# Performance work log

Measured on AMD Instinct MI355X. Metric: run time of the kernel, lower is better.

Reference implementation:

```python
import jax, jax.numpy as jnp
from jax import lax
import numpy as np

B, N = 32, 16384
C, K = 64, 21
T = 30
L = 10.0
LAM = 0.1


def setup_inputs() -> dict:
    key = jax.random.key(0)
    k1, k2 = jax.random.split(key)
    y = jax.random.normal(k1, (B, 1, N), dtype=jnp.float32)
    H = jax.random.normal(k2, (C, 1, K), dtype=jnp.float32)
    H = H / jnp.linalg.norm(H, axis=-1, keepdims=True)  # F.normalize(p=2, dim=-1)
    return {"y": y, "H": H}


def _conv(y, H):
    # torch F.conv1d(y [B,1,N], H [C,1,K]) -> [B,C,N-K+1] (cross-correlation)
    return lax.conv_general_dilated(y, H, (1,), 'VALID',
                                    dimension_numbers=('NCH', 'OIH', 'NCH'))


def _convT(x, H):
    # torch F.conv_transpose1d(x [B,C,M], H [C,1,K]) -> [B,1,M+K-1]
    k = H.shape[-1]
    Ht = jnp.transpose(jnp.flip(H, -1), (1, 0, 2))  # [1,C,K] OIH, flipped
    return lax.conv_general_dilated(x, Ht, (1,), [(k - 1, k - 1)],
                                    dimension_numbers=('NCH', 'OIH', 'NCH'))


def reference(y, H):
    enc_dim = y.shape[-1] - H.shape[-1] + 1  # N - K + 1
    b = y.shape[0]
    c = H.shape[0]
    x0 = jnp.zeros((b, c, enc_dim), dtype=y.dtype)
    s0 = jnp.asarray(1.0, dtype=y.dtype)

    def step(carry, _):
        x_old, x_tmp, s_old = carry
        res = y - _convT(x_tmp, H)                      # residual [B,1,N]
        x_new = x_tmp + _conv(res, H) / L               # gradient step
        x_new = jax.nn.relu(x_new - LAM / L)            # soft-threshold (nonneg)
        s_new = (1.0 + jnp.sqrt(1.0 + 4.0 * s_old * s_old)) / 2.0
        x_tmp_next = x_new + (s_old - 1.0) / s_new * (x_new - x_old)
        return (x_new, x_tmp_next, s_new), None

    (x_new, _, _), _ = lax.scan(step, (x0, x0, s0), None, length=T)
    y_hat = _convT(x_new, H)
    return (y_hat, x_new)
```

## Files before the change

kernel.cpp:

```cpp
#include <hip/hip_runtime.h>
#include <math.h>

#define B_ 32
#define N_ 16384
#define K_ 21
#define C_ 64
#define M_ (N_ - K_ + 1)
#define T_ 30

#define TILE 236
#define NBLK 70
#define UPW  256
#define NT   256

__global__ __launch_bounds__(NT) void fused_step4_kernel(
    const float* __restrict__ Xc, const float* __restrict__ Xo,
    float* __restrict__ Xw,
    const float* __restrict__ Ut, const float* __restrict__ Uo,
    float* __restrict__ Uw,
    const float* __restrict__ y, const float* __restrict__ Hg,
    const float bp, const float bm, const int first)
{
  __shared__ float rs[280];
  __shared__ float rp[4][256];

  const int tid = threadIdx.x;
  const int wv  = tid >> 6;
  const int l   = tid & 63;
  const int b   = blockIdx.y;
  const int x   = blockIdx.x;
  const int m0  = x * TILE;
  const bool has_o = (bm != 0.f);

  if (tid < 24) rs[256 + tid] = 0.f;

  {
    const int n = m0 + tid;
    float r = 0.f;
    if (n < N_) {
      r = y[(size_t)b * N_ + n];
      if (!first) {
        const float* Ub = Ut + (size_t)b * NBLK * UPW;
        float ut;
        if (tid >= 236) {
          ut = Ub[(x + 1) * UPW + tid - 236] + Ub[x * UPW + tid];
        } else {
          ut = Ub[x * UPW + tid];
          if (tid < 20 && x > 0) ut += Ub[(x - 1) * UPW + 236 + tid];
        }
        r -= bp * ut;
        if (has_o) {
          const float* Vb = Uo + (size_t)b * NBLK * UPW;
          float uo;
          if (tid >= 236) {
            uo = Vb[(x + 1) * UPW + tid - 236] + Vb[x * UPW + tid];
          } else {
            uo = Vb[x * UPW + tid];
            if (tid < 20 && x > 0) uo += Vb[(x - 1) * UPW + 236 + tid];
          }
          r -= bm * uo;
        }
      }
    }
    rs[tid] = r;
  }
  __syncthreads();

  float wr[24];
  #pragma unroll
  for (int kk = 0; kk < 6; ++kk) {
    const float4 v = *(const float4*)&rs[(l << 2) + (kk << 2)];
    wr[4*kk+0] = v.x; wr[4*kk+1] = v.y;
    wr[4*kk+2] = v.z; wr[4*kk+3] = v.w;
  }

  const int  mown = m0 + (l << 2);
  const int  coff = (mown <= M_ - 4) ? mown : (M_ - 4);
  const bool act  = (l < 59) && ((l << 2) < M_ - m0);
  const size_t bC = (size_t)b * C_;

  float p0 = 0.f, p1 = 0.f, p2 = 0.f, p3 = 0.f;

  for (int k = 0; k < 4; ++k) {
    #pragma unroll
    for (int j = 0; j < 4; ++j) {
      const int cg = __builtin_amdgcn_readfirstlane((k << 4) + (wv << 2) + j);
      const float* hc = Hg + cg * K_;

      float g0 = 0.f, g1 = 0.f, g2 = 0.f, g3 = 0.f;
      #pragma unroll
      for (int u = 0; u < 21; ++u) {
        const float hv = hc[u];
        g0 = fmaf(wr[u],     hv, g0);
        g1 = fmaf(wr[u + 1], hv, g1);
        g2 = fmaf(wr[u + 2], hv, g2);
        g3 = fmaf(wr[u + 3], hv, g3);
      }

      float xt0 = 0.f, xt1 = 0.f, xt2 = 0.f, xt3 = 0.f;
      if (!first) {
        const float4 a = *(const float4*)(Xc + (bC + cg) * M_ + coff);
        float ox = 0.f, oy = 0.f, oz = 0.f, ow = 0.f;
        if (has_o) {
          const float4 o = *(const float4*)(Xo + (bC + cg) * M_ + coff);
          ox = o.x; oy = o.y; oz = o.z; ow = o.w;
        }
        xt0 = fmaf(bm, ox, bp * a.x);
        xt1 = fmaf(bm, oy, bp * a.y);
        xt2 = fmaf(bm, oz, bp * a.z);
        xt3 = fmaf(bm, ow, bp * a.w);
      }

      float o0 = fmaxf(fmaf(g0, 0.1f, xt0) - 0.01f, 0.f);
      float o1 = fmaxf(fmaf(g1, 0.1f, xt1) - 0.01f, 0.f);
      float o2 = fmaxf(fmaf(g2, 0.1f, xt2) - 0.01f, 0.f);
      float o3 = fmaxf(fmaf(g3, 0.1f, xt3) - 0.01f, 0.f);
      if (!act) { o0 = 0.f; o1 = 0.f; o2 = 0.f; o3 = 0.f; }
      if (act)
        *(float4*)(Xw + (bC + cg) * M_ + mown) = make_float4(o0, o1, o2, o3);

      float w[24];
      w[20] = o0; w[21] = o1; w[22] = o2; w[23] = o3;
      #pragma unroll
      for (int d = 0; d < 5; ++d) {
        const int src = l - 5 + d;
        w[4*d+0] = __shfl(o0, src);
        w[4*d+1] = __shfl(o1, src);
        w[4*d+2] = __shfl(o2, src);
        w[4*d+3] = __shfl(o3, src);
      }

      #pragma unroll
      for (int u = 0; u < 21; ++u) {
        const float hv = hc[20 - u];
        p0 = fmaf(w[u],     hv, p0);
        p1 = fmaf(w[u + 1], hv, p1);
        p2 = fmaf(w[u + 2], hv, p2);
        p3 = fmaf(w[u + 3], hv, p3);
      }
    }
  }

  rp[wv][(l<<2)+0] = p0; rp[wv][(l<<2)+1] = p1;
  rp[wv][(l<<2)+2] = p2; rp[wv][(l<<2)+3] = p3;
  __syncthreads();

  Uw[((size_t)b * NBLK + x) * UPW + tid] =
      rp[0][tid] + rp[1][tid] + rp[2][tid] + rp[3][tid];
}

__global__ __launch_bounds__(NT) void yhat_combine_kernel(
    const float* __restrict__ Uw, float* __restrict__ outy)
{
  const int tid = threadIdx.x;
  const int n = blockIdx.x * 256 + tid;
  const int b = blockIdx.y;
  const int x = n / 236;
  const int i = n - x * 236;
  const float* Ub = Uw + (size_t)b * NBLK * UPW;
  float v = Ub[x * UPW + i];
  if (i < 20 && x > 0) v += Ub[(x - 1) * UPW + 236 + i];
  outy[(size_t)b * N_ + n] = v;
}

#define XWID 276
#define Q4PC 69
#define NQ4  (16 * Q4PC)

__global__ __launch_bounds__(NT, 4) void fused_step_r5_kernel(
    const float* __restrict__ Xc, const float* __restrict__ Xo,
    float* __restrict__ Xw, const float* __restrict__ y,
    const float* __restrict__ Hg, const float bp, const float bm,
    const int first)
{
  __shared__ float xs[16][XWID];
  __shared__ float rp[4][256];
  __shared__ float rs[256];

  const int tid = threadIdx.x;
  const int wv  = tid >> 6;
  const int l   = tid & 63;
  const int b   = blockIdx.y;
  const int m0  = blockIdx.x * TILE;
  const int g0  = m0 - 20;
  const bool has_o = (bm != 0.f);

  if (!first) {
    float p0 = 0.f, p1 = 0.f, p2 = 0.f, p3 = 0.f;
    for (int k = 0; k < 4; ++k) {
      const int ch0 = k << 4;
      const float* pcb = Xc + ((size_t)b * C_ + ch0) * M_;
      const float* pob = Xo + ((size_t)b * C_ + ch0) * M_;
      __syncthreads();
      for (int f = tid; f < NQ4; f += NT) {
        const int c  = f / Q4PC;
        const int i4 = f - c * Q4PC;
        const int g  = g0 + (i4 << 2);
        const float* pa = pcb + (size_t)c * M_ + g;
        const float* pb = pob + (size_t)c * M_ + g;
        float ax, ay, az, aw, ox, oy, oz, ow;
        if (g >= 0 && g + 3 < M_) {
          const float4 a = *(const float4*)pa;
          ax = a.x; ay = a.y; az = a.z; aw = a.w;
          if (has_o) {
            const float4 o = *(const float4*)pb;
            ox = o.x; oy = o.y; oz = o.z; ow = o.w;
          } else { ox = oy = oz = ow = 0.f; }
        } else {
          ax = ay = az = aw = ox = oy = oz = ow = 0.f;
          if ((unsigned)(g+0) < (unsigned)M_) { ax = pa[0]; if (has_o) ox = pb[0]; }
          if ((unsigned)(g+1) < (unsigned)M_) { ay = pa[1]; if (has_o) oy = pb[1]; }
          if ((unsigned)(g+2) < (unsigned)M_) { az = pa[2]; if (has_o) oz = pb[2]; }
          if ((unsigned)(g+3) < (unsigned)M_) { aw = pa[3]; if (has_o) ow = pb[3]; }
        }
        float4 w4;
        w4.x = fmaf(bm, ox, bp * ax);
        w4.y = fmaf(bm, oy, bp * ay);
        w4.z = fmaf(bm, oz, bp * az);
        w4.w = fmaf(bm, ow, bp * aw);
        *(float4*)&xs[c][i4 << 2] = w4;
      }
      __syncthreads();
      #pragma unroll
      for (int j = 0; j < 4; ++j) {
        const int cloc = (wv << 2) + j;
        const int cg = __builtin_amdgcn_readfirstlane(ch0 + cloc);
        const float* hc = Hg + cg * K_;
        float w[24];
        #pragma unroll
        for (int kk = 0; kk < 6; ++kk) {
          const float4 v = *(const float4*)&xs[cloc][(l << 2) + (kk << 2)];
          w[4*kk+0] = v.x; w[4*kk+1] = v.y;
          w[4*kk+2] = v.z; w[4*kk+3] = v.w;
        }
        #pragma unroll
        for (int u = 0; u < 21; ++u) {
          const float hv = hc[20 - u];
          p0 = fmaf(w[u],     hv, p0);
          p1 = fmaf(w[u + 1], hv, p1);
          p2 = fmaf(w[u + 2], hv, p2);
          p3 = fmaf(w[u + 3], hv, p3);
        }
      }
    }
    *(float4*)&rp[wv][l << 2] = make_float4(p0, p1, p2, p3);
  }
  __syncthreads();

  {
    const int n = m0 + tid;
    float r = 0.f;
    if (n < N_) {
      r = y[(size_t)b * N_ + n];
      if (!first) r -= rp[0][tid] + rp[1][tid] + rp[2][tid] + rp[3][tid];
    }
    rs[tid] = r;
  }
  __syncthreads();

  if (l < 59 && (l << 2) < M_ - m0) {
    float wr[24];
    #pragma unroll
    for (int kk = 0; kk < 6; ++kk) {
      const float4 v = *(const float4*)&rs[(l << 2) + (kk << 2)];
      wr[4*kk+0] = v.x; wr[4*kk+1] = v.y;
      wr[4*kk+2] = v.z; wr[4*kk+3] = v.w;
    }
    #pragma unroll 4
    for (int cl = 0; cl < 16; ++cl) {
      const int cg = __builtin_amdgcn_readfirstlane((wv << 4) + cl);
      const size_t row = ((size_t)b * C_ + cg) * M_ + m0 + (l << 2);
      float xt0, xt1, xt2, xt3;
      if (!first) {
        const float4 a = *(const float4*)(Xc + row);
        float ox = 0.f, oy = 0.f, oz = 0.f, ow = 0.f;
        if (has_o) {
          const float4 o = *(const float4*)(Xo + row);
          ox = o.x; oy = o.y; oz = o.z; ow = o.w;
        }
        xt0 = fmaf(bm, ox, bp * a.x);
        xt1 = fmaf(bm, oy, bp * a.y);
        xt2 = fmaf(bm, oz, bp * a.z);
        xt3 = fmaf(bm, ow, bp * a.w);
      } else { xt0 = xt1 = xt2 = xt3 = 0.f; }
      const float* hc = Hg + cg * K_;
      float a0 = 0.f, a1 = 0.f, a2 = 0.f, a3 = 0.f;
      #pragma unroll
      for (int u = 0; u < 21; ++u) {
        const float hv = hc[u];
        a0 = fmaf(wr[u],     hv, a0);
        a1 = fmaf(wr[u + 1], hv, a1);
        a2 = fmaf(wr[u + 2], hv, a2);
        a3 = fmaf(wr[u + 3], hv, a3);
      }
      const float o0 = fmaxf(fmaf(a0, 0.1f, xt0) - 0.01f, 0.f);
      const float o1 = fmaxf(fmaf(a1, 0.1f, xt1) - 0.01f, 0.f);
      const float o2 = fmaxf(fmaf(a2, 0.1f, xt2) - 0.01f, 0.f);
      const float o3 = fmaxf(fmaf(a3, 0.1f, xt3) - 0.01f, 0.f);
      *(float4*)(Xw + row) = make_float4(o0, o1, o2, o3);
    }
  }
}

#define TA 1024
#define CC 16

__global__ __launch_bounds__(NT) void convT_kernel(
    const float* __restrict__ X, const float* __restrict__ y,
    const float* __restrict__ Hg, float* __restrict__ out,
    const int use_y, const float sign)
{
  __shared__ float xs[CC][TA + 20];
  __shared__ float hs[C_][K_];
  const int tid = threadIdx.x;
  const int b = blockIdx.y;
  const int n0 = blockIdx.x * TA;

  for (int f = tid; f < C_ * K_; f += NT) hs[f / K_][f % K_] = sign * Hg[f];

  float acc[4];
  if (use_y) {
    const float4 v = *(const float4*)(y + (size_t)b * N_ + n0 + tid * 4);
    acc[0] = v.x; acc[1] = v.y; acc[2] = v.z; acc[3] = v.w;
  } else {
    acc[0] = acc[1] = acc[2] = acc[3] = 0.f;
  }
  const bool interior = (n0 >= 20) && (n0 + TA - 1 <= M_ - 1);
  const int QROW = (TA + 20) / 4;
  for (int cb = 0; cb < C_; cb += CC) {
    __syncthreads();
    for (int f = tid; f < CC * QROW; f += NT) {
      const int c = f / QROW;
      const int i = (f % QROW) * 4;
      const int gx = n0 - 20 + i;
      const float* src = X + ((size_t)(b * C_ + cb + c)) * M_ + gx;
      float4 v;
      if (interior) {
        v = *(const float4*)src;
      } else {
        v.x = (gx >= 0     && gx < M_)     ? src[0] : 0.f;
        v.y = (gx + 1 >= 0 && gx + 1 < M_) ? src[1] : 0.f;
        v.z = (gx + 2 >= 0 && gx + 2 < M_) ? src[2] : 0.f;
        v.w = (gx + 3 >= 0 && gx + 3 < M_) ? src[3] : 0.f;
      }
      *(float4*)&xs[c][i] = v;
    }
    __syncthreads();
    for (int c = 0; c < CC; ++c) {
      float w[24];
      #pragma unroll
      for (int k = 0; k < 6; ++k) {
        const float4 v = *(const float4*)&xs[c][tid * 4 + k * 4];
        w[k*4] = v.x; w[k*4+1] = v.y; w[k*4+2] = v.z; w[k*4+3] = v.w;
      }
      const float* hr = hs[cb + c];
      #pragma unroll
      for (int j = 0; j < K_; ++j) {
        const float h = hr[j];
        acc[0] = fmaf(h, w[20 - j], acc[0]);
        acc[1] = fmaf(h, w[21 - j], acc[1]);
        acc[2] = fmaf(h, w[22 - j], acc[2]);
        acc[3] = fmaf(h, w[23 - j], acc[3]);
      }
    }
  }
  *(float4*)(out + (size_t)b * N_ + n0 + tid * 4) =
      make_float4(acc[0], acc[1], acc[2], acc[3]);
}

extern "C" void kernel_launch(void* const* d_in, const int* in_sizes, int n_in,
                              void* d_out, int out_size, void* d_ws, size_t ws_size,
                              hipStream_t stream)
{
  const float* y = (const float*)d_in[0];
  const float* H = (const float*)d_in[1];
  float* out  = (float*)d_out;
  float* outy = out;
  float* outx = out + (size_t)B_ * N_;

  const size_t SZ = (size_t)B_ * C_ * M_;
  const size_t UP = (size_t)B_ * NBLK * UPW;

  float betas[T_];
  double s = 1.0;
  for (int t = 0; t < T_; ++t) {
    const double sn = (1.0 + sqrt(1.0 + 4.0 * s * s)) * 0.5;
    betas[t] = (float)((s - 1.0) / sn);
    s = sn;
  }

  const dim3 blk(NT);

  if (ws_size >= (2 * SZ + 3 * UP) * sizeof(float)) {
    float* XB[2] = { outx, (float*)d_ws };
    float* U[3]  = { (float*)d_ws + 2 * SZ,
                     (float*)d_ws + 2 * SZ + UP,
                     (float*)d_ws + 2 * SZ + 2 * UP };
    const dim3 gF(NBLK, B_);
    for (int t = 0; t < T_; ++t) {
      const float beta = (t >= 1) ? betas[t - 1] : 0.f;
      const float* Xc = XB[t & 1];
      const float* Xo = (beta != 0.f) ? XB[(t + 1) & 1] : Xc;
      float*       Xw = XB[(t + 1) & 1];
      const float* Ut = U[(t + 2) % 3];
      const float* Uo = (beta != 0.f) ? U[(t + 1) % 3] : U[(t + 2) % 3];
      float*       Uw = U[t % 3];
      fused_step4_kernel<<<gF, blk, 0, stream>>>(
          Xc, Xo, Xw, Ut, Uo, Uw, y, H, 1.f + beta, -beta, t == 0);
    }
    const dim3 gY(N_ / 256, B_);
    yhat_combine_kernel<<<gY, blk, 0, stream>>>(U[(T_ - 1) % 3], outy);
  } else {
    float* P[3] = { (float*)d_ws, (float*)d_ws + SZ, outx };
    const dim3 gF((M_ + TILE - 1) / TILE, B_);
    for (int t = 0; t < T_; ++t) {
      const float beta = (t >= 1) ? betas[t - 1] : 0.f;
      const float* Xc = P[(t + 2) % 3];
      const float* Xo = (beta != 0.f) ? P[(t + 1) % 3] : P[(t + 2) % 3];
      float*       Xw = P[t % 3];
      fused_step_r5_kernel<<<gF, blk, 0, stream>>>(Xc, Xo, Xw, y, H,
                                                   1.f + beta, -beta, t == 0);
    }
    const dim3 gA(N_ / TA, B_);
    convT_kernel<<<gA, blk, 0, stream>>>(outx, y, H, outy, 0, 1.f);
  }
}
```

Baseline: 2.706 ms.

## Fuse all FISTA iterations into one cooperative persistent kernel with grid sync

Replaces the 30 per-iteration kernel launches plus the final combine launch with a single cooperative kernel. It loops over timesteps internally, assigns tiles to persistent blocks and separates iterations with grid.sync(). The goal is to remove launch overhead and the inter-kernel gaps. In exchange each iteration pays for a grid-wide barrier, and grid size is capped by occupancy, which may leave compute units with uneven tile counts. Falls back to the old multi-launch path if cooperative launch is unavailable.

New measurement: 2.661 ms. No clear change (-1.7%).

```diff
diff --git a/kernel.cpp b/kernel.cpp
--- a/kernel.cpp
+++ b/kernel.cpp
@@ -1,5 +1,8 @@
 #include <hip/hip_runtime.h>
+#include <hip/hip_cooperative_groups.h>
 #include <math.h>
+
+namespace cg = cooperative_groups;
 
 #define B_ 32
 #define N_ 16384
@@ -13,22 +16,19 @@
 #define UPW  256
 #define NT   256
 
-__global__ __launch_bounds__(NT) void fused_step4_kernel(
+__device__ __forceinline__ void step_tile(
     const float* __restrict__ Xc, const float* __restrict__ Xo,
     float* __restrict__ Xw,
     const float* __restrict__ Ut, const float* __restrict__ Uo,
     float* __restrict__ Uw,
     const float* __restrict__ y, const float* __restrict__ Hg,
-    const float bp, const float bm, const int first)
-{
-  __shared__ float rs[280];
-  __shared__ float rp[4][256];
-
+    const float bp, const float bm, const int first,
+    const int b, const int x,
+    float* __restrict__ rs, float* __restrict__ rpf)
+{
   const int tid = threadIdx.x;
   const int wv  = tid >> 6;
   const int l   = tid & 63;
-  const int b   = blockIdx.y;
-  const int x   = blockIdx.x;
   const int m0  = x * TILE;
   const bool has_o = (bm != 0.f);
 
@@ -84,8 +84,8 @@
   for (int k = 0; k < 4; ++k) {
     #pragma unroll
     for (int j = 0; j < 4; ++j) {
-      const int cg = __builtin_amdgcn_readfirstlane((k << 4) + (wv << 2) + j);
-      const float* hc = Hg + cg * K_;
+      const int cg_ = __builtin_amdgcn_readfirstlane((k << 4) + (wv << 2) + j);
+      const float* hc = Hg + cg_ * K_;
 
       float g0 = 0.f, g1 = 0.f, g2 = 0.f, g3 = 0.f;
       #pragma unroll
@@ -99,10 +99,10 @@
 
       float xt0 = 0.f, xt1 = 0.f, xt2 = 0.f, xt3 = 0.f;
       if (!first) {
-        const float4 a = *(const float4*)(Xc + (bC + cg) * M_ + coff);
+        const float4 a = *(const float4*)(Xc + (bC + cg_) * M_ + coff);
         float ox = 0.f, oy = 0.f, oz = 0.f, ow = 0.f;
         if (has_o) {
-          const float4 o = *(const float4*)(Xo + (bC + cg) * M_ + coff);
+          const float4 o = *(const float4*)(Xo + (bC + cg_) * M_ + coff);
           ox = o.x; oy = o.y; oz = o.z; ow = o.w;
         }
         xt0 = fmaf(bm, ox, bp * a.x);
@@ -117,7 +117,7 @@
       float o3 = fmaxf(fmaf(g3, 0.1f, xt3) - 0.01f, 0.f);
       if (!act) { o0 = 0.f; o1 = 0.f; o2 = 0.f; o3 = 0.f; }
       if (act)
-        *(float4*)(Xw + (bC + cg) * M_ + mown) = make_float4(o0, o1, o2, o3);
+        *(float4*)(Xw + (bC + cg_) * M_ + mown) = make_float4(o0, o1, o2, o3);
 
       float w[24];
       w[20] = o0; w[21] = o1; w[22] = o2; w[23] = o3;
@@ -141,12 +141,77 @@
     }
   }
 
-  rp[wv][(l<<2)+0] = p0; rp[wv][(l<<2)+1] = p1;
-  rp[wv][(l<<2)+2] = p2; rp[wv][(l<<2)+3] = p3;
+  rpf[(wv << 8) + (l << 2) + 0] = p0;
+  rpf[(wv << 8) + (l << 2) + 1] = p1;
+  rpf[(wv << 8) + (l << 2) + 2] = p2;
+  rpf[(wv << 8) + (l << 2) + 3] = p3;
   __syncthreads();
 
   Uw[((size_t)b * NBLK + x) * UPW + tid] =
-      rp[0][tid] + rp[1][tid] + rp[2][tid] + rp[3][tid];
+      rpf[tid] + rpf[256 + tid] + rpf[512 + tid] + rpf[768 + tid];
+}
+
+struct CoopArgs {
+  const float* y; const float* Hg;
+  float* x0; float* x1;
+  float* u0; float* u1; float* u2;
+  float* outy;
+  float bp[T_]; float bm[T_];
+};
+
+__global__ __launch_bounds__(NT) void fista_coop_kernel(CoopArgs a)
+{
+  __shared__ float rs[280];
+  __shared__ float rp[4 * 256];
+  cg::grid_group grid = cg::this_grid();
+
+  float* XB[2] = { a.x0, a.x1 };
+  float* U[3]  = { a.u0, a.u1, a.u2 };
+
+  for (int t = 0; t < T_; ++t) {
+    const float bp = a.bp[t], bm = a.bm[t];
+    const int first = (t == 0);
+    const float* Xc = XB[t & 1];
+    float*       Xw = XB[(t + 1) & 1];
+    const float* Xo = (bm != 0.f) ? XB[(t + 1) & 1] : Xc;
+    const float* Ut = U[(t + 2) % 3];
+    const float* Uo = (bm != 0.f) ? U[(t + 1) % 3] : U[(t + 2) % 3];
+    float*       Uw = U[t % 3];
+
+    for (int tile = blockIdx.x; tile < B_ * NBLK; tile += gridDim.x) {
+      const int b = tile / NBLK;
+      const int x = tile - b * NBLK;
+      step_tile(Xc, Xo, Xw, Ut, Uo, Uw, a.y, a.Hg, bp, bm, first, b, x,
+                rs, rp);
+    }
+    grid.sync();
+  }
+
+  const float* Uf = U[(T_ - 1) % 3];
+  for (int tile = blockIdx.x; tile < 64 * B_; tile += gridDim.x) {
+    const int b = tile >> 6;
+    const int n = ((tile & 63) << 8) + threadIdx.x;
+    const int xq = n / 236;
+    const int i  = n - xq * 236;
+    const float* Ub = Uf + (size_t)b * NBLK * UPW;
+    float v = Ub[xq * UPW + i];
+    if (i < 20 && xq > 0) v += Ub[(xq - 1) * UPW + 236 + i];
+    a.outy[(size_t)b * N_ + n] = v;
+  }
+}
+
+__global__ __launch_bounds__(NT) void fused_step4_kernel(
+    const float* __restrict__ Xc, const float* __restrict__ Xo,
+    float* __restrict__ Xw,
+    const float* __restrict__ Ut, const float* __restrict__ Uo,
+    float* __restrict__ Uw,
+    const float* __restrict__ y, const float* __restrict__ Hg,
+    const float bp, const float bm, const int first)
+{
+  __shared__ float rs[280];
+  __shared__ float rp[4 * 256];
+  step_tile(Xc, Xo, Xw, Ut, Uo, Uw, y, Hg, bp, bm, first,
+            blockIdx.y, blockIdx.x, rs, rp);
 }
 
 __global__ __launch_bounds__(NT) void yhat_combine_kernel(
@@ -224,8 +289,8 @@
       #pragma unroll
       for (int j = 0; j < 4; ++j) {
         const int cloc = (wv << 2) + j;
-        const int cg = __builtin_amdgcn_readfirstlane(ch0 + cloc);
-        const float* hc = Hg + cg * K_;
+        const int cg_ = __builtin_amdgcn_readfirstlane(ch0 + cloc);
+        const float* hc = Hg + cg_ * K_;
         float w[24];
         #pragma unroll
         for (int kk = 0; kk < 6; ++kk) {
@@ -268,8 +333,8 @@
     }
     #pragma unroll 4
     for (int cl = 0; cl < 16; ++cl) {
-      const int cg = __builtin_amdgcn_readfirstlane((wv << 4) + cl);
-      const size_t row = ((size_t)b * C_ + cg) * M_ + m0 + (l << 2);
+      const int cg_ = __builtin_amdgcn_readfirstlane((wv << 4) + cl);
+      const size_t row = ((size_t)b * C_ + cg_) * M_ + m0 + (l << 2);
       float xt0, xt1, xt2, xt3;
       if (!first) {
         const float4 a = *(const float4*)(Xc + row);
@@ -283,7 +348,7 @@
         xt2 = fmaf(bm, oz, bp * a.z);
         xt3 = fmaf(bm, ow, bp * a.w);
       } else { xt0 = xt1 = xt2 = xt3 = 0.f; }
-      const float* hc = Hg + cg * K_;
+      const float* hc = Hg + cg_ * K_;
       float a0 = 0.f, a1 = 0.f, a2 = 0.f, a3 = 0.f;
       #pragma unroll
       for (int u = 0; u < 21; ++u) {
@@ -390,12 +455,44 @@
   }
 
   const dim3 blk(NT);
-
-  if (ws_size >= (2 * SZ + 3 * UP) * sizeof(float)) {
+  const bool big_ws = ws_size >= (2 * SZ + 3 * UP) * sizeof(float);
+
+  if (big_ws) {
     float* XB[2] = { outx, (float*)d_ws };
     float* U[3]  = { (float*)d_ws + 2 * SZ,
                      (float*)d_ws + 2 * SZ + UP,
                      (float*)d_ws + 2 * SZ + 2 * UP };
+
+    int dev = 0, coopAttr = 0, ncu = 0, maxb = 0;
+    bool coop = (hipGetDevice(&dev) == hipSuccess);
+    if (coop) coop = (hipDeviceGetAttribute(&coopAttr,
+                        hipDeviceAttributeCooperativeLaunch, dev) == hipSuccess)
+                     && coopAttr;
+    if (coop) coop = (hipDeviceGetAttribute(&ncu,
+                        hipDeviceAttributeMultiprocessorCount, dev) == hipSuccess)
+                     && ncu > 0;
+    if (coop) coop = (hipOccupancyMaxActiveBlocksPerMultiprocessor(
+                        &maxb, fista_coop_kernel, NT, 0) == hipSuccess)
+                     && maxb >= 1;
+    if (coop) {
+      int blocks = ncu * (maxb > 8 ? 8 : maxb);
+      if (blocks > B_ * NBLK) blocks = B_ * NBLK;
+      CoopArgs a;
+      a.y = y; a.Hg = H;
+      a.x0 = XB[0]; a.x1 = XB[1];
+      a.u0 = U[0]; a.u1 = U[1]; a.u2 = U[2];
+      a.outy = outy;
+      for (int t = 0; t < T_; ++t) {
+        const float beta = (t >= 1) ? betas[t - 1] : 0.f;
+        a.bp[t] = 1.f + beta;
+        a.bm[t] = -beta;
+      }
+      void* kp[1] = { (void*)&a };
+      if (hipLaunchCooperativeKernel(fista_coop_kernel, dim3(blocks), blk,
+                                     kp, 0, stream) == hipSuccess)
+        return;
+    }
+
     const dim3 gF(NBLK, B_);
     for (int t = 0; t < T_; ++t) {
       const float beta = (t >= 1) ? betas[t - 1] : 0.f;
```
